# Performance work log

Hardware: AMD Instinct MI355X
Metric: run time of the kernel (lower is better)

The kernel has to match this reference:

```python
import jax, jax.numpy as jnp
import numpy as np

B, S, IN, OUT, E, K = 4, 2048, 4096, 4096, 8, 16
POOLS = E * K  # 128 rank-one pools


def setup_inputs() -> dict:
    key = jax.random.key(0)
    k1, k2, k3, k4, k5 = jax.random.split(key, 5)
    sc = 0.02
    return {
        "hidden_states": jax.random.normal(k1, (B, S, IN), jnp.float32),
        "w0": jax.random.normal(k2, (OUT, IN), jnp.float32) * sc,   # pretrained Linear weight
        "b0": jnp.zeros((OUT,), jnp.float32),                        # pretrained Linear bias
        "wr": jax.random.normal(k3, (POOLS, IN), jnp.float32) * sc,  # Router stacked v.T
        "u": jax.random.normal(k4, (OUT, POOLS), jnp.float32) * sc,  # RankOnePools.u
        "svh": jax.random.normal(k5, (POOLS, IN), jnp.float32) * sc, # RankOnePools.svh
        "top_k": 2,
    }


def reference(hidden_states, w0, b0, wr, u, svh, top_k):
    # pretrained dense path (expert_use_diff=True)
    pretrained_out = jnp.einsum('bsi,oi->bso', hidden_states, w0) + b0

    x = hidden_states.reshape(-1, hidden_states.shape[-1])  # [N, IN]

    # Router: logits over num_experts*k rank-one pools
    logits = jnp.einsum('ni,pi->np', x, wr)                  # [N, POOLS]
    vals, idx = jax.lax.top_k(logits, top_k)                 # [N, top_k]
    vals = vals / jnp.sum(vals, axis=-1, keepdims=True)      # computed but UNUSED (matches original torch code)

    # RankOnePools: gather selected rank-one factors and combine
    svh_sel = svh[idx]                                       # [N, top_k, IN]
    dot = jnp.einsum('ni,nti->nt', x, svh_sel)               # [N, top_k]
    u_sel = u.T[idx]                                         # [N, top_k, OUT]
    expert_out = jnp.einsum('nt,nto->no', dot, u_sel)        # [N, OUT]

    out = pretrained_out + expert_out.reshape(pretrained_out.shape)
    return out
```

## Files before the change

### kernel.cpp

```cpp
#include <hip/hip_runtime.h>

#define K_DIM  4096
#define N_OUT  4096
#define N_TOK  8192
#define N_POOL 128

typedef __bf16 bf16x8 __attribute__((ext_vector_type(8)));
typedef float  f32x4  __attribute__((ext_vector_type(4)));
typedef unsigned short u16x8 __attribute__((ext_vector_type(8)));

__device__ __forceinline__ unsigned short f2bf(float f) {
    union { float f; unsigned u; } v; v.f = f;
    unsigned r = v.u + 0x7fffu + ((v.u >> 16) & 1u);
    return (unsigned short)(r >> 16);
}
__device__ __forceinline__ float bf2f(unsigned short b) {
    union { unsigned u; float f; } v; v.u = ((unsigned)b) << 16;
    return v.f;
}

__global__ __launch_bounds__(256) void k_convert_w0(const float* __restrict__ w0,
                                                    unsigned short* __restrict__ w0b) {
    size_t base = ((size_t)blockIdx.x * 256 + threadIdx.x) * 8;
    float4 a = *(const float4*)(w0 + base);
    float4 b = *(const float4*)(w0 + base + 4);
    u16x8 r;
    r[0] = f2bf(a.x); r[1] = f2bf(a.y); r[2] = f2bf(a.z); r[3] = f2bf(a.w);
    r[4] = f2bf(b.x); r[5] = f2bf(b.y); r[6] = f2bf(b.z); r[7] = f2bf(b.w);
    *(u16x8*)(w0b + base) = r;
}

__global__ __launch_bounds__(256) void k_split_wr(const float* __restrict__ wr,
                                                  unsigned short* __restrict__ wrh,
                                                  unsigned short* __restrict__ wrl) {
    size_t base = ((size_t)blockIdx.x * 256 + threadIdx.x) * 4;
    float4 a = *(const float4*)(wr + base);
    ushort4 h, l;
    h.x = f2bf(a.x); h.y = f2bf(a.y); h.z = f2bf(a.z); h.w = f2bf(a.w);
    l.x = f2bf(a.x - bf2f(h.x)); l.y = f2bf(a.y - bf2f(h.y));
    l.z = f2bf(a.z - bf2f(h.z)); l.w = f2bf(a.w - bf2f(h.w));
    *(ushort4*)(wrh + base) = h;
    *(ushort4*)(wrl + base) = l;
}

__global__ __launch_bounds__(256) void k_transpose_u(const float* __restrict__ u,
                                                     float* __restrict__ uT) {
    __shared__ float t[32][65];
    const int o0 = blockIdx.x * 64, p0 = blockIdx.y * 32;
    const int tid = threadIdx.x;
#pragma unroll
    for (int it = 0; it < 8; it++) {
        int o = (tid >> 5) + it * 8;
        t[tid & 31][o] = u[(size_t)(o0 + o) * N_POOL + p0 + (tid & 31)];
    }
    __syncthreads();
#pragma unroll
    for (int it = 0; it < 8; it++) {
        int p = (tid >> 6) + it * 4;
        uT[(size_t)(p0 + p) * N_OUT + o0 + (tid & 63)] = t[p][tid & 63];
    }
}

#define RTK 64
#define TAU 0.01f

__global__ __launch_bounds__(512) void k_router(const float* __restrict__ x,
                                                const float* __restrict__ wr,
                                                const unsigned short* __restrict__ wrh,
                                                const unsigned short* __restrict__ wrl,
                                                const float* __restrict__ svh,
                                                unsigned short* __restrict__ xb,
                                                int* __restrict__ idxp,
                                                float* __restrict__ dotp) {
    __shared__ __attribute__((aligned(16))) unsigned short Ah[32 * RTK];
    __shared__ __attribute__((aligned(16))) unsigned short Al[32 * RTK];
    __shared__ __attribute__((aligned(16))) unsigned short Bh[N_POOL * RTK];
    __shared__ __attribute__((aligned(16))) unsigned short Bl[N_POOL * RTK];
    __shared__ float lg[32][N_POOL + 1];
    __shared__ float thr2[32];
    __shared__ int   flg[32];
    __shared__ int   sel[32][2];

    const int tid  = threadIdx.x;
    const int lane = tid & 63;
    const int w    = tid >> 6;
    const int wm   = w & 1;
    const int wn   = w >> 1;
    const int lrow = lane & 15, lquad = lane >> 4;
    const size_t m0 = (size_t)blockIdx.x * 32;

    const int atok  = tid >> 4;
    const int akoff = (tid & 15) * 4;
    const int aswz  = ((((tid & 15) >> 1) ^ (atok & 7)) * 8) + (tid & 1) * 4;

    const int brow = tid >> 3;

    float4 x_pf = *(const float4*)(x + (m0 + atok) * K_DIM + akoff);

    f32x4 acc[2] = {};

    for (int k0 = 0; k0 < K_DIM; k0 += RTK) {
        __syncthreads();
        {
            ushort4 h, l;
            h.x = f2bf(x_pf.x); h.y = f2bf(x_pf.y); h.z = f2bf(x_pf.z); h.w = f2bf(x_pf.w);
            l.x = f2bf(x_pf.x - bf2f(h.x)); l.y = f2bf(x_pf.y - bf2f(h.y));
            l.z = f2bf(x_pf.z - bf2f(h.z)); l.w = f2bf(x_pf.w - bf2f(h.w));
            *(ushort4*)(xb + (m0 + atok) * K_DIM + k0 + akoff) = h;
            *(ushort4*)(&Ah[atok * RTK + aswz]) = h;
            *(ushort4*)(&Al[atok * RTK + aswz]) = l;
        }
#pragma unroll
        for (int i = 0; i < 2; i++) {
            const int r = brow + i * 64;
            const int c = (tid & 7) ^ (r & 7);
            __builtin_amdgcn_global_load_lds(
                (const __attribute__((address_space(1))) void*)(wrh + (size_t)r * K_DIM + k0 + c * 8),
                (__attribute__((address_space(3))) void*)(Bh + i * 4096 + tid * 8), 16, 0, 0);
            __builtin_amdgcn_global_load_lds(
                (const __attribute__((address_space(1))) void*)(wrl + (size_t)r * K_DIM + k0 + c * 8),
                (__attribute__((address_space(3))) void*)(Bl + i * 4096 + tid * 8), 16, 0, 0);
        }
        __syncthreads();
        if (k0 + RTK < K_DIM)
            x_pf = *(const float4*)(x + (m0 + atok) * K_DIM + k0 + RTK + akoff);
#pragma unroll
        for (int ks = 0; ks < 2; ks++) {
            const int cs = ((ks * 4 + lquad) ^ (lrow & 7)) * 8;
            bf16x8 ah = *(const bf16x8*)&Ah[(wm * 16 + lrow) * RTK + cs];
            bf16x8 al = *(const bf16x8*)&Al[(wm * 16 + lrow) * RTK + cs];
#pragma unroll
            for (int nt = 0; nt < 2; nt++) {
                bf16x8 bh = *(const bf16x8*)&Bh[(wn * 32 + nt * 16 + lrow) * RTK + cs];
                bf16x8 bl = *(const bf16x8*)&Bl[(wn * 32 + nt * 16 + lrow) * RTK + cs];
                acc[nt] = __builtin_amdgcn_mfma_f32_16x16x32_bf16(ah, bh, acc[nt], 0, 0, 0);
                acc[nt] = __builtin_amdgcn_mfma_f32_16x16x32_bf16(ah, bl, acc[nt], 0, 0, 0);
                acc[nt] = __builtin_amdgcn_mfma_f32_16x16x32_bf16(al, bh, acc[nt], 0, 0, 0);
            }
        }
    }

#pragma unroll
    for (int nt = 0; nt < 2; nt++)
#pragma unroll
        for (int r = 0; r < 4; r++)
            lg[wm * 16 + lquad * 4 + r][wn * 32 + nt * 16 + lrow] = acc[nt][r];
    __syncthreads();

    if (tid < 32) {
        float v1 = -3.4e38f, v2 = -3.4e38f, v3 = -3.4e38f; int i1 = 0, i2 = 0;
        for (int p = 0; p < N_POOL; p++) {
            float v = lg[tid][p];
            if (v > v1)      { v3 = v2; v2 = v1; i2 = i1; v1 = v; i1 = p; }
            else if (v > v2) { v3 = v2; v2 = v;  i2 = p; }
            else if (v > v3) { v3 = v; }
        }
        sel[tid][0] = i1; sel[tid][1] = i2;
        thr2[tid] = v2 - TAU;
        flg[tid]  = (v2 - v3 < TAU) ? 1 : 0;
    }
    __syncthreads();

    if (w == 0) {
        for (int s = 0; s < 32; s++) {
            if (!flg[s]) continue;
            const float th = thr2[s];
            unsigned long long c0 = __ballot(lg[s][lane] >= th);
            unsigned long long c1 = __ballot(lg[s][64 + lane] >= th);
            float v1 = -3.4e38f, v2 = -3.4e38f; int i1 = 0, i2 = 0;
            const float* xr = x + (m0 + s) * K_DIM;
            for (int half = 0; half < 2; half++) {
                unsigned long long m = half ? c1 : c0;
                while (m) {
                    const int p = (half ? 64 : 0) + __ffsll(m) - 1;
                    m &= m - 1;
                    const float* wp = wr + (size_t)p * K_DIM;
                    float d = 0.f;
#pragma unroll 8
                    for (int it = 0; it < 64; it++)
                        d += xr[it * 64 + lane] * wp[it * 64 + lane];
#pragma unroll
                    for (int off = 32; off > 0; off >>= 1) d += __shfl_down(d, off);
                    d = __shfl(d, 0);
                    if (d > v1)      { v2 = v1; i2 = i1; v1 = d; i1 = p; }
                    else if (d > v2) { v2 = d; i2 = p; }
                }
            }
            if (lane == 0) { sel[s][0] = i1; sel[s][1] = i2; }
        }
    }
    __syncthreads();

    if (tid < 32) {
        idxp[(m0 + tid) * 2 + 0] = sel[tid][0];
        idxp[(m0 + tid) * 2 + 1] = sel[tid][1];
    }

    for (int s = w; s < 32; s += 8) {
        const size_t n = m0 + s;
        const int e0 = sel[s][0], e1 = sel[s][1];
        float d0 = 0.f, d1 = 0.f;
#pragma unroll
        for (int it = 0; it < 8; it++) {
            const int e = (it * 64 + lane) * 8;
            u16x8 xv = *(const u16x8*)(xb + n * K_DIM + e);
            float4 s0 = *(const float4*)(svh + (size_t)e0 * K_DIM + e);
            float4 s1 = *(const float4*)(svh + (size_t)e0 * K_DIM + e + 4);
            float4 s2 = *(const float4*)(svh + (size_t)e1 * K_DIM + e);
            float4 s3 = *(const float4*)(svh + (size_t)e1 * K_DIM + e + 4);
            float x0 = bf2f(xv[0]), x1 = bf2f(xv[1]), x2 = bf2f(xv[2]), x3 = bf2f(xv[3]);
            float x4 = bf2f(xv[4]), x5 = bf2f(xv[5]), x6 = bf2f(xv[6]), x7 = bf2f(xv[7]);
            d0 += x0*s0.x + x1*s0.y + x2*s0.z + x3*s0.w + x4*s1.x + x5*s1.y + x6*s1.z + x7*s1.w;
            d1 += x0*s2.x + x1*s2.y + x2*s2.z + x3*s2.w + x4*s3.x + x5*s3.y + x6*s3.z + x7*s3.w;
        }
#pragma unroll
        for (int off = 32; off > 0; off >>= 1) {
            d0 += __shfl_down(d0, off);
            d1 += __shfl_down(d1, off);
        }
        if (lane == 0) { dotp[n * 2 + 0] = d0; dotp[n * 2 + 1] = d1; }
    }
}

__global__ __launch_bounds__(256) void k_gemm(const unsigned short* __restrict__ xb,
                                              const unsigned short* __restrict__ w0b,
                                              const float* __restrict__ b0,
                                              const float* __restrict__ uT,
                                              const int* __restrict__ idxp,
                                              const float* __restrict__ dotp,
                                              float* __restrict__ out) {
    __shared__ unsigned short Als[128 * 64];
    __shared__ unsigned short Bls[128 * 64];

    const int tid  = threadIdx.x;
    const int lane = tid & 63;
    const int wv   = tid >> 6;
    const int wm   = wv & 1, wn = wv >> 1;
    const int lrow = lane & 15, lquad = lane >> 4;
    const size_t m0 = (size_t)blockIdx.y * 128;
    const size_t n0 = (size_t)blockIdx.x * 128;

    const int srow   = tid >> 3;
    const int xchunk = (tid & 7) ^ (srow & 7);
    const unsigned short* ag = xb  + (m0 + srow) * K_DIM + xchunk * 8;
    const unsigned short* bg = w0b + (n0 + srow) * K_DIM + xchunk * 8;
    unsigned short* al = Als + tid * 8;
    unsigned short* bl = Bls + tid * 8;

    f32x4 acc[4][4] = {};

    for (int k0 = 0; k0 < K_DIM; k0 += 64) {
        __syncthreads();
#pragma unroll
        for (int i = 0; i < 4; i++) {
            __builtin_amdgcn_global_load_lds(
                (const __attribute__((address_space(1))) void*)(ag + (size_t)i * 32 * K_DIM + k0),
                (__attribute__((address_space(3))) void*)(al + i * 2048), 16, 0, 0);
            __builtin_amdgcn_global_load_lds(
                (const __attribute__((address_space(1))) void*)(bg + (size_t)i * 32 * K_DIM + k0),
                (__attribute__((address_space(3))) void*)(bl + i * 2048), 16, 0, 0);
        }
        __syncthreads();
#pragma unroll
        for (int ks = 0; ks < 2; ks++) {
            bf16x8 af[4], bfr[4];
#pragma unroll
            for (int t = 0; t < 4; t++)
                af[t] = *(const bf16x8*)&Als[(wm * 64 + t * 16 + lrow) * 64 +
                                             (((ks * 4 + lquad) ^ (lrow & 7)) * 8)];
#pragma unroll
            for (int t = 0; t < 4; t++)
                bfr[t] = *(const bf16x8*)&Bls[(wn * 64 + t * 16 + lrow) * 64 +
                                              (((ks * 4 + lquad) ^ (lrow & 7)) * 8)];
#pragma unroll
            for (int mt = 0; mt < 4; mt++)
#pragma unroll
                for (int nt = 0; nt < 4; nt++)
                    acc[mt][nt] = __builtin_amdgcn_mfma_f32_16x16x32_bf16(af[mt], bfr[nt], acc[mt][nt], 0, 0, 0);
        }
    }

#pragma unroll
    for (int mt = 0; mt < 4; mt++) {
        const size_t rb = m0 + wm * 64 + mt * 16 + lquad * 4;
#pragma unroll
        for (int r = 0; r < 4; r++) {
            const size_t gm = rb + r;
            const int e0 = idxp[gm * 2 + 0], e1 = idxp[gm * 2 + 1];
            const float dd0 = dotp[gm * 2 + 0], dd1 = dotp[gm * 2 + 1];
#pragma unroll
            for (int nt = 0; nt < 4; nt++) {
                const size_t gn = n0 + wn * 64 + nt * 16 + lrow;
                float vv = acc[mt][nt][r] + b0[gn]
                         + dd0 * uT[(size_t)e0 * N_OUT + gn] + dd1 * uT[(size_t)e1 * N_OUT + gn];
                out[gm * N_OUT + gn] = vv;
            }
        }
    }
}

extern "C" void kernel_launch(void* const* d_in, const int* in_sizes, int n_in,
                              void* d_out, int out_size, void* d_ws, size_t ws_size,
                              hipStream_t stream) {
    const float* x   = (const float*)d_in[0];
    const float* w0  = (const float*)d_in[1];
    const float* b0  = (const float*)d_in[2];
    const float* wr  = (const float*)d_in[3];
    const float* u   = (const float*)d_in[4];
    const float* svh = (const float*)d_in[5];
    float* out = (float*)d_out;

    char* ws = (char*)d_ws;
    unsigned short* xb  = (unsigned short*)ws;
    unsigned short* w0b = (unsigned short*)(ws + 67108864);
    int*   idxp = (int*)(ws + 100663296);
    float* dotp = (float*)(ws + 100663296 + 65536);
    float* uTp  = (float*)(ws + 100663296 + 131072);
    unsigned short* wrh = (unsigned short*)(ws + 102891520);
    unsigned short* wrl = (unsigned short*)(ws + 103940096);

    k_convert_w0<<<dim3(16777216 / (256 * 8)), dim3(256), 0, stream>>>(w0, w0b);
    k_split_wr<<<dim3(N_POOL * K_DIM / (256 * 4)), dim3(256), 0, stream>>>(wr, wrh, wrl);
    k_transpose_u<<<dim3(N_OUT / 64, N_POOL / 32), dim3(256), 0, stream>>>(u, uTp);
    k_router<<<dim3(N_TOK / 32), dim3(512), 0, stream>>>(x, wr, wrh, wrl, svh, xb, idxp, dotp);
    k_gemm<<<dim3(N_OUT / 128, N_TOK / 128), dim3(256), 0, stream>>>(xb, w0b, b0, uTp, idxp, dotp, out);
}
```

Baseline: 692.5 us.

## Double-buffer GEMM tiles at 256x256 with 512 threads and swizzled block order

The main bf16 GEMM moves from 128x128 tiles with 4 waves and single-buffered LDS to 256x256 tiles with 8 waves. Async global-to-LDS loads are double-buffered and synchronised with explicit vmcnt waits and barriers, so the next K-slice loads while the current one is computed. Block IDs are remapped to spread tiles across the grid for better L2 reuse. The larger tile cuts global traffic per FLOP, but uses 128 KB of LDS and 128 accumulator registers per lane, which limits occupancy and shrinks the grid to 512 blocks.

```diff
diff --git a/kernel.cpp b/kernel.cpp
--- a/kernel.cpp
+++ b/kernel.cpp
@@ -222,67 +222,91 @@
     }
 }
 
-__global__ __launch_bounds__(256) void k_gemm(const unsigned short* __restrict__ xb,
+__global__ __launch_bounds__(512) void k_gemm(const unsigned short* __restrict__ xb,
                                               const unsigned short* __restrict__ w0b,
                                               const float* __restrict__ b0,
                                               const float* __restrict__ uT,
                                               const int* __restrict__ idxp,
                                               const float* __restrict__ dotp,
                                               float* __restrict__ out) {
-    __shared__ unsigned short Als[128 * 64];
-    __shared__ unsigned short Bls[128 * 64];
+    __shared__ __attribute__((aligned(16))) unsigned short Als[2][256 * 64];
+    __shared__ __attribute__((aligned(16))) unsigned short Bls[2][256 * 64];
 
     const int tid  = threadIdx.x;
     const int lane = tid & 63;
-    const int wv   = tid >> 6;
-    const int wm   = wv & 1, wn = wv >> 1;
+    const int w    = tid >> 6;
+    const int wm   = w >> 2, wn = w & 3;
     const int lrow = lane & 15, lquad = lane >> 4;
-    const size_t m0 = (size_t)blockIdx.y * 128;
-    const size_t n0 = (size_t)blockIdx.x * 128;
+
+    const int lg = (blockIdx.x & 7) * 64 + (blockIdx.x >> 3);
+    const size_t n0 = (size_t)(lg & 15) * 256;
+    const size_t m0 = (size_t)(lg >> 4) * 256;
 
     const int srow   = tid >> 3;
     const int xchunk = (tid & 7) ^ (srow & 7);
     const unsigned short* ag = xb  + (m0 + srow) * K_DIM + xchunk * 8;
     const unsigned short* bg = w0b + (n0 + srow) * K_DIM + xchunk * 8;
-    unsigned short* al = Als + tid * 8;
-    unsigned short* bl = Bls + tid * 8;
-
-    f32x4 acc[4][4] = {};
-
-    for (int k0 = 0; k0 < K_DIM; k0 += 64) {
-        __syncthreads();
-#pragma unroll
-        for (int i = 0; i < 4; i++) {
-            __builtin_amdgcn_global_load_lds(
-                (const __attribute__((address_space(1))) void*)(ag + (size_t)i * 32 * K_DIM + k0),
-                (__attribute__((address_space(3))) void*)(al + i * 2048), 16, 0, 0);
-            __builtin_amdgcn_global_load_lds(
-                (const __attribute__((address_space(1))) void*)(bg + (size_t)i * 32 * K_DIM + k0),
-                (__attribute__((address_space(3))) void*)(bl + i * 2048), 16, 0, 0);
-        }
-        __syncthreads();
-#pragma unroll
-        for (int ks = 0; ks < 2; ks++) {
-            bf16x8 af[4], bfr[4];
-#pragma unroll
-            for (int t = 0; t < 4; t++)
-                af[t] = *(const bf16x8*)&Als[(wm * 64 + t * 16 + lrow) * 64 +
-                                             (((ks * 4 + lquad) ^ (lrow & 7)) * 8)];
-#pragma unroll
-            for (int t = 0; t < 4; t++)
-                bfr[t] = *(const bf16x8*)&Bls[(wn * 64 + t * 16 + lrow) * 64 +
-                                              (((ks * 4 + lquad) ^ (lrow & 7)) * 8)];
-#pragma unroll
-            for (int mt = 0; mt < 4; mt++)
-#pragma unroll
-                for (int nt = 0; nt < 4; nt++)
-                    acc[mt][nt] = __builtin_amdgcn_mfma_f32_16x16x32_bf16(af[mt], bfr[nt], acc[mt][nt], 0, 0, 0);
-        }
-    }
-
-#pragma unroll
-    for (int mt = 0; mt < 4; mt++) {
-        const size_t rb = m0 + wm * 64 + mt * 16 + lquad * 4;
+
+    f32x4 acc[8][4] = {};
+
+#define STAGE(buf, k0)                                                                        \
+    {                                                                                         \
+        unsigned short* al = &Als[buf][tid * 8];                                              \
+        unsigned short* bl = &Bls[buf][tid * 8];                                              \
+        _Pragma("unroll")                                                                     \
+        for (int l = 0; l < 4; l++) {                                                         \
+            __builtin_amdgcn_global_load_lds(                                                 \
+                (const __attribute__((address_space(1))) void*)(ag + (size_t)l * 64 * K_DIM + (k0)), \
+                (__attribute__((address_space(3))) void*)(al + l * 4096), 16, 0, 0);          \
+            __builtin_amdgcn_global_load_lds(                                                 \
+                (const __attribute__((address_space(1))) void*)(bg + (size_t)l * 64 * K_DIM + (k0)), \
+                (__attribute__((address_space(3))) void*)(bl + l * 4096), 16, 0, 0);          \
+        }                                                                                     \
+    }
+
+#define COMPUTE(buf)                                                                          \
+    {                                                                                         \
+        _Pragma("unroll")                                                                     \
+        for (int ks = 0; ks < 2; ks++) {                                                      \
+            const int cs = ((ks * 4 + lquad) ^ (lrow & 7)) * 8;                               \
+            bf16x8 bfv[4];                                                                    \
+            _Pragma("unroll")                                                                 \
+            for (int nt = 0; nt < 4; nt++)                                                    \
+                bfv[nt] = *(const bf16x8*)&Bls[buf][(wn * 64 + nt * 16 + lrow) * 64 + cs];    \
+            _Pragma("unroll")                                                                 \
+            for (int mt = 0; mt < 8; mt++) {                                                  \
+                bf16x8 av = *(const bf16x8*)&Als[buf][(wm * 128 + mt * 16 + lrow) * 64 + cs]; \
+                _Pragma("unroll")                                                             \
+                for (int nt = 0; nt < 4; nt++)                                                \
+                    acc[mt][nt] = __builtin_amdgcn_mfma_f32_16x16x32_bf16(av, bfv[nt], acc[mt][nt], 0, 0, 0); \
+            }                                                                                 \
+        }                                                                                     \
+    }
+
+    STAGE(0, 0)
+    STAGE(1, 64)
+
+    for (int t = 0; t < 63; ++t) {
+        asm volatile("s_waitcnt vmcnt(8)" ::: "memory");
+        __builtin_amdgcn_s_barrier();
+        const int buf = t & 1;
+        COMPUTE(buf)
+        __builtin_amdgcn_s_barrier();
+        if (t < 62) STAGE(buf, (t + 2) * 64)
+    }
+    asm volatile("s_waitcnt vmcnt(0)" ::: "memory");
+    __builtin_amdgcn_s_barrier();
+    COMPUTE(1)
+
+#undef STAGE
+#undef COMPUTE
+
+    float b0v[4];
+#pragma unroll
+    for (int nt = 0; nt < 4; nt++) b0v[nt] = b0[n0 + wn * 64 + nt * 16 + lrow];
+#pragma unroll
+    for (int mt = 0; mt < 8; mt++) {
+        const size_t rb = m0 + wm * 128 + mt * 16 + lquad * 4;
 #pragma unroll
         for (int r = 0; r < 4; r++) {
             const size_t gm = rb + r;
@@ -291,7 +315,7 @@
 #pragma unroll
             for (int nt = 0; nt < 4; nt++) {
                 const size_t gn = n0 + wn * 64 + nt * 16 + lrow;
-                float vv = acc[mt][nt][r] + b0[gn]
+                float vv = acc[mt][nt][r] + b0v[nt]
                          + dd0 * uT[(size_t)e0 * N_OUT + gn] + dd1 * uT[(size_t)e1 * N_OUT + gn];
                 out[gm * N_OUT + gn] = vv;
             }
@@ -323,5 +347,5 @@
     k_split_wr<<<dim3(N_POOL * K_DIM / (256 * 4)), dim3(256), 0, stream>>>(wr, wrh, wrl);
     k_transpose_u<<<dim3(N_OUT / 64, N_POOL / 32), dim3(256), 0, stream>>>(u, uTp);
     k_router<<<dim3(N_TOK / 32), dim3(512), 0, stream>>>(x, wr, wrh, wrl, svh, xb, idxp, dotp);
-    k_gemm<<<dim3(N_OUT / 128, N_TOK / 128), dim3(256), 0, stream>>>(xb, w0b, b0, uTp, idxp, dotp, out);
-}
+    k_gemm<<<dim3(512), dim3(512), 0, stream>>>(xb, w0b, b0, uTp, idxp, dotp, out);
+}
```

Measured after the change: 680.9 us. No clear change (-1.7%).
